# Optimization experiments

Measured on AMD Instinct MI355X. Metric: run time of the kernel, lower is better.

Reference implementation:

```python
import jax, jax.numpy as jnp
import numpy as np

DIM = 64; NFEATS = 32; DEPTH = 4; HEADS = 8; DIM_HEAD = 64
INNER = HEADS * DIM_HEAD            # 512
DI_COL = int(DIM * 4.0)             # 256
D_ROW = DIM * NFEATS                # 2048
DI_ROW = int(D_ROW * 0.5)           # 1024
B = 2048; NCAT = 16; NCONT = 16
EPS = 1e-5


def setup_inputs() -> dict:
    key = jax.random.key(0)
    ks = iter(jax.random.split(key, 32))
    def w(shape):
        return jax.random.normal(next(ks), shape, jnp.float32) * 0.02
    inp = {
        'x': jax.random.normal(next(ks), (B, NCAT, DIM), jnp.float32),
        'x_cont': jax.random.normal(next(ks), (B, NCONT, DIM), jnp.float32),
        # col-attention blocks (stacked over depth)
        'c_ln1_g': jnp.ones((DEPTH, DIM), jnp.float32),
        'c_ln1_b': jnp.zeros((DEPTH, DIM), jnp.float32),
        'c_wqkv': w((DEPTH, DIM, 3 * INNER)),
        'c_wo_w': w((DEPTH, INNER, DIM)),
        'c_wo_b': jnp.zeros((DEPTH, DIM), jnp.float32),
        'c_ln2_g': jnp.ones((DEPTH, DIM), jnp.float32),
        'c_ln2_b': jnp.zeros((DEPTH, DIM), jnp.float32),
        'c_w1': w((DEPTH, DIM, 2 * DI_COL)),
        'c_b1': jnp.zeros((DEPTH, 2 * DI_COL), jnp.float32),
        'c_w2': w((DEPTH, DI_COL, DIM)),
        'c_b2': jnp.zeros((DEPTH, DIM), jnp.float32),
        # row (intersample) blocks
        'r_ln1_g': jnp.ones((DEPTH, D_ROW), jnp.float32),
        'r_ln1_b': jnp.zeros((DEPTH, D_ROW), jnp.float32),
        'r_wqkv': w((DEPTH, D_ROW, 3 * INNER)),
        'r_wo_w': w((DEPTH, INNER, D_ROW)),
        'r_wo_b': jnp.zeros((DEPTH, D_ROW), jnp.float32),
        'r_ln2_g': jnp.ones((DEPTH, D_ROW), jnp.float32),
        'r_ln2_b': jnp.zeros((DEPTH, D_ROW), jnp.float32),
        'r_w1': w((DEPTH, D_ROW, 2 * DI_ROW)),
        'r_b1': jnp.zeros((DEPTH, 2 * DI_ROW), jnp.float32),
        'r_w2': w((DEPTH, DI_ROW, D_ROW)),
        'r_b2': jnp.zeros((DEPTH, D_ROW), jnp.float32),
    }
    return inp


def _ln(x, g, b):
    m = x.mean(-1, keepdims=True)
    v = ((x - m) ** 2).mean(-1, keepdims=True)
    return (x - m) / jnp.sqrt(v + EPS) * g + b


def _attn(x, wqkv, wo_w, wo_b):
    b, n, _ = x.shape
    q, k, v = jnp.split(x @ wqkv, 3, axis=-1)
    sp = lambda t: t.reshape(b, n, HEADS, DIM_HEAD).transpose(0, 2, 1, 3)
    q, k, v = sp(q), sp(k), sp(v)
    logits = jnp.einsum('bhid,bhjd->bhij', q, k) * (DIM_HEAD ** -0.5)
    a = jax.nn.softmax(logits, axis=-1)
    o = jnp.einsum('bhij,bhjd->bhid', a, v)
    o = o.transpose(0, 2, 1, 3).reshape(b, n, INNER)
    return o @ wo_w + wo_b


def _geglu_mlp(x, w1, b1, w2, b2):
    h = x @ w1 + b1
    a, g = jnp.split(h, 2, axis=-1)
    return (a * jax.nn.gelu(g, approximate=False)) @ w2 + b2


def _block(x, ln1g, ln1b, wqkv, wow, wob, ln2g, ln2b, w1, b1, w2, b2):
    # PreNorm(Residual(fn)): out = fn(LN(x)) + LN(x)  (residual on normalized x)
    xn = _ln(x, ln1g, ln1b)
    x = _attn(xn, wqkv, wow, wob) + xn
    xn = _ln(x, ln2g, ln2b)
    return _geglu_mlp(xn, w1, b1, w2, b2) + xn


def reference(x, x_cont,
              c_ln1_g, c_ln1_b, c_wqkv, c_wo_w, c_wo_b, c_ln2_g, c_ln2_b, c_w1, c_b1, c_w2, c_b2,
              r_ln1_g, r_ln1_b, r_wqkv, r_wo_w, r_wo_b, r_ln2_g, r_ln2_b, r_w1, r_b1, r_w2, r_b2):
    x = jnp.concatenate([x, x_cont], axis=1)  # [B, NFEATS, DIM]
    for i in range(DEPTH):
        # col: attention over features within each sample
        x = _block(x, c_ln1_g[i], c_ln1_b[i], c_wqkv[i], c_wo_w[i], c_wo_b[i],
                   c_ln2_g[i], c_ln2_b[i], c_w1[i], c_b1[i], c_w2[i], c_b2[i])
        # row: intersample attention, 'b n d -> 1 b (n d)'
        xr = x.reshape(1, B, D_ROW)
        xr = _block(xr, r_ln1_g[i], r_ln1_b[i], r_wqkv[i], r_wo_w[i], r_wo_b[i],
                    r_ln2_g[i], r_ln2_b[i], r_w1[i], r_b1[i], r_w2[i], r_b2[i])
        x = xr.reshape(B, NFEATS, DIM)
    return x
```

## Files before the change

### kernel.cpp

```cpp
#include <hip/hip_runtime.h>
#include <hip/hip_bf16.h>
#include <cstddef>

#define BD    2048
#define NF    32
#define DIMC  64
#define HEADS 8
#define DROW  2048
#define LNEPS 1e-5f

typedef __hip_bfloat16 bf16;
typedef __attribute__((ext_vector_type(8))) short short8;
typedef __attribute__((ext_vector_type(4))) float f32x4;

#define MFMA16 __builtin_amdgcn_mfma_f32_16x16x32_bf16

__device__ inline float ldin(const void* p, size_t i, int bf) {
    if (bf) return __bfloat162float(((const bf16*)p)[i]);
    return ((const float*)p)[i];
}

__device__ inline float gelu_exact(float x) {
    return 0.5f * x * (1.0f + erff(x * 0.70710678118654752f));
}

__global__ __launch_bounds__(64) void k_detect(const void* __restrict__ x,
                                               int* __restrict__ flag) {
    int i = threadIdx.x;
    size_t idx = (size_t)(2 * i) * 16384;
    unsigned short u = ((const unsigned short*)x)[idx];
    int e = (u >> 7) & 0xFF;
    int plausible = (e == 0) || (e >= 96 && e <= 132);
    unsigned long long m = __ballot(plausible);
    if (i == 0) *flag = (__popcll(m) >= 48) ? 1 : 0;
}

__global__ __launch_bounds__(256) void k_concat(const void* __restrict__ x,
                                                const void* __restrict__ xc,
                                                float* __restrict__ X,
                                                const int* __restrict__ flag) {
    const int bf = *flag;
    int i = blockIdx.x * 256 + threadIdx.x;
    int d = i & 63;
    int f = (i >> 6) & 31;
    int b = i >> 11;
    float v = (f < 16) ? ldin(x,  ((size_t)b * 16 + f) * 64 + d, bf)
                       : ldin(xc, ((size_t)b * 16 + (f - 16)) * 64 + d, bf);
    X[i] = v;
}

__global__ __launch_bounds__(256) void k_ln64(const float* __restrict__ in,
                                              float* __restrict__ out,
                                              bf16* __restrict__ outh,
                                              const void* __restrict__ g,
                                              const void* __restrict__ b,
                                              size_t eoff,
                                              const int* __restrict__ flag) {
    const int bf = *flag;
    int row  = blockIdx.x * 4 + (threadIdx.x >> 6);
    int lane = threadIdx.x & 63;
    float v = in[(size_t)row * 64 + lane];
    float s = v;
    #pragma unroll
    for (int off = 32; off; off >>= 1) s += __shfl_xor(s, off);
    float mean = s * (1.0f / 64.0f);
    float dx = v - mean;
    float s2 = dx * dx;
    #pragma unroll
    for (int off = 32; off; off >>= 1) s2 += __shfl_xor(s2, off);
    float inv = rsqrtf(s2 * (1.0f / 64.0f) + LNEPS);
    float o = dx * inv * ldin(g, eoff + lane, bf) + ldin(b, eoff + lane, bf);
    out[(size_t)row * 64 + lane]  = o;
    outh[(size_t)row * 64 + lane] = __float2bfloat16(o);
}

__global__ __launch_bounds__(256) void k_ln_row(const float* __restrict__ in,
                                                float* __restrict__ out,
                                                bf16* __restrict__ outh,
                                                const void* __restrict__ g,
                                                const void* __restrict__ b,
                                                size_t eoff,
                                                const int* __restrict__ flag) {
    const int bf = *flag;
    const int row = blockIdx.x, tid = threadIdx.x;
    __shared__ float red[4];
    const float* r = in + (size_t)row * DROW;
    float v[8];
    float s = 0.f;
    #pragma unroll
    for (int i = 0; i < 8; ++i) { v[i] = r[tid + i * 256]; s += v[i]; }
    #pragma unroll
    for (int off = 32; off; off >>= 1) s += __shfl_xor(s, off);
    if ((tid & 63) == 0) red[tid >> 6] = s;
    __syncthreads();
    float mean = (red[0] + red[1] + red[2] + red[3]) * (1.0f / DROW);
    __syncthreads();
    float s2 = 0.f;
    #pragma unroll
    for (int i = 0; i < 8; ++i) { float dx = v[i] - mean; s2 += dx * dx; }
    #pragma unroll
    for (int off = 32; off; off >>= 1) s2 += __shfl_xor(s2, off);
    if ((tid & 63) == 0) red[tid >> 6] = s2;
    __syncthreads();
    float inv = rsqrtf((red[0] + red[1] + red[2] + red[3]) * (1.0f / DROW) + LNEPS);
    #pragma unroll
    for (int i = 0; i < 8; ++i) {
        int j = tid + i * 256;
        float o = (v[i] - mean) * inv * ldin(g, eoff + j, bf) + ldin(b, eoff + j, bf);
        out[(size_t)row * DROW + j]  = o;
        outh[(size_t)row * DROW + j] = __float2bfloat16(o);
    }
}

__global__ __launch_bounds__(256) void k_castT(const void* __restrict__ in, size_t eoff,
                                               int R, int C,
                                               bf16* __restrict__ out,
                                               const int* __restrict__ flag) {
    const int bf = *flag;
    __shared__ bf16 tile[32][33];
    const int tx = threadIdx.x & 31, ty = threadIdx.x >> 5;
    const int bx = blockIdx.x, by = blockIdx.y;
    #pragma unroll
    for (int k = 0; k < 4; ++k) {
        int r = bx * 32 + ty + k * 8;
        int c = by * 32 + tx;
        tile[ty + k * 8][tx] = __float2bfloat16(ldin(in, eoff + (size_t)r * C + c, bf));
    }
    __syncthreads();
    #pragma unroll
    for (int k = 0; k < 4; ++k) {
        int oc = by * 32 + ty + k * 8;
        int orr = bx * 32 + tx;
        out[(size_t)oc * R + orr] = tile[tx][ty + k * 8];
    }
}

__global__ __launch_bounds__(256) void k_transpose_bf(const bf16* __restrict__ in, int ld,
                                                      int R, int C,
                                                      bf16* __restrict__ out) {
    __shared__ bf16 tile[32][33];
    const int tx = threadIdx.x & 31, ty = threadIdx.x >> 5;
    const int bx = blockIdx.x, by = blockIdx.y;
    #pragma unroll
    for (int k = 0; k < 4; ++k) {
        int r = bx * 32 + ty + k * 8;
        int c = by * 32 + tx;
        tile[ty + k * 8][tx] = in[(size_t)r * ld + c];
    }
    __syncthreads();
    #pragma unroll
    for (int k = 0; k < 4; ++k) {
        int oc = by * 32 + ty + k * 8;
        int orr = bx * 32 + tx;
        out[(size_t)oc * R + orr] = tile[tx][ty + k * 8];
    }
}

template <int WM, int WN, bool OBF>
__global__ __launch_bounds__(256) void k_mfma(
    int M, int N, int K,
    const bf16* __restrict__ A, int lda, long long sA,
    const bf16* __restrict__ Bt, int ldb, long long sB,
    void* __restrict__ C, int ldc, long long sC,
    float alpha,
    const void* __restrict__ bias, size_t biasOff,
    const float* __restrict__ addend, int ldadd,
    const int* __restrict__ flag)
{
    constexpr int TM = WM * 64, TN = WN * 64;
    const int z = blockIdx.z;
    A  += (size_t)z * sA;
    Bt += (size_t)z * sB;
    const int m0 = blockIdx.y * TM, n0 = blockIdx.x * TN;
    const int tid = threadIdx.x, lane = tid & 63, wave = tid >> 6;
    const int wy = wave / WN, wx = wave % WN;
    __shared__ short As[TM][72];
    __shared__ short Bs[TN][72];
    f32x4 acc[4][4] = {};
    const int row8 = tid >> 3, chunk = (tid & 7) * 8;
    for (int k0 = 0; k0 < K; k0 += 64) {
        #pragma unroll
        for (int i = 0; i < TM / 32; ++i) {
            int r = i * 32 + row8;
            *(short8*)&As[r][chunk] =
                *(const short8*)(A + (size_t)(m0 + r) * lda + k0 + chunk);
        }
        #pragma unroll
        for (int i = 0; i < TN / 32; ++i) {
            int r = i * 32 + row8;
            *(short8*)&Bs[r][chunk] =
                *(const short8*)(Bt + (size_t)(n0 + r) * ldb + k0 + chunk);
        }
        __syncthreads();
        #pragma unroll
        for (int ks = 0; ks < 64; ks += 32) {
            short8 af[4], bfr[4];
            #pragma unroll
            for (int mt = 0; mt < 4; ++mt)
                af[mt] = *(const short8*)&As[wy * 64 + mt * 16 + (lane & 15)][ks + (lane >> 4) * 8];
            #pragma unroll
            for (int nt = 0; nt < 4; ++nt)
                bfr[nt] = *(const short8*)&Bs[wx * 64 + nt * 16 + (lane & 15)][ks + (lane >> 4) * 8];
            #pragma unroll
            for (int mt = 0; mt < 4; ++mt)
                #pragma unroll
                for (int nt = 0; nt < 4; ++nt)
                    acc[mt][nt] = MFMA16(af[mt], bfr[nt], acc[mt][nt], 0, 0, 0);
        }
        __syncthreads();
    }
    const int bfl = bias ? *flag : 0;
    #pragma unroll
    for (int mt = 0; mt < 4; ++mt) {
        #pragma unroll
        for (int r = 0; r < 4; ++r) {
            int m = m0 + wy * 64 + mt * 16 + (lane >> 4) * 4 + r;
            #pragma unroll
            for (int nt = 0; nt < 4; ++nt) {
                int n = n0 + wx * 64 + nt * 16 + (lane & 15);
                float v = acc[mt][nt][r] * alpha;
                if (bias)   v += ldin(bias, biasOff + n, bfl);
                if (addend) v += addend[(size_t)m * ldadd + n];
                size_t idx = (size_t)z * sC + (size_t)m * ldc + n;
                if constexpr (OBF) ((bf16*)C)[idx] = __float2bfloat16(v);
                else               ((float*)C)[idx] = v;
            }
        }
    }
}

template <int WM, int WN>
__global__ __launch_bounds__(256) void k_mfma_sk(
    int M, int N, int KC,
    const bf16* __restrict__ A, int lda,
    const bf16* __restrict__ Bt, int ldb,
    float* __restrict__ Cp, long long pstride)
{
    constexpr int TM = WM * 64, TN = WN * 64;
    const int z = blockIdx.z;
    const int m0 = blockIdx.y * TM, n0 = blockIdx.x * TN;
    const int tid = threadIdx.x, lane = tid & 63, wave = tid >> 6;
    const int wy = wave / WN, wx = wave % WN;
    __shared__ short As[TM][72];
    __shared__ short Bs[TN][72];
    f32x4 acc[4][4] = {};
    const int row8 = tid >> 3, chunk = (tid & 7) * 8;
    const int kend = z * KC + KC;
    for (int k0 = z * KC; k0 < kend; k0 += 64) {
        #pragma unroll
        for (int i = 0; i < TM / 32; ++i) {
            int r = i * 32 + row8;
            *(short8*)&As[r][chunk] =
                *(const short8*)(A + (size_t)(m0 + r) * lda + k0 + chunk);
        }
        #pragma unroll
        for (int i = 0; i < TN / 32; ++i) {
            int r = i * 32 + row8;
            *(short8*)&Bs[r][chunk] =
                *(const short8*)(Bt + (size_t)(n0 + r) * ldb + k0 + chunk);
        }
        __syncthreads();
        #pragma unroll
        for (int ks = 0; ks < 64; ks += 32) {
            short8 af[4], bfr[4];
            #pragma unroll
            for (int mt = 0; mt < 4; ++mt)
                af[mt] = *(const short8*)&As[wy * 64 + mt * 16 + (lane & 15)][ks + (lane >> 4) * 8];
            #pragma unroll
            for (int nt = 0; nt < 4; ++nt)
                bfr[nt] = *(const short8*)&Bs[wx * 64 + nt * 16 + (lane & 15)][ks + (lane >> 4) * 8];
            #pragma unroll
            for (int mt = 0; mt < 4; ++mt)
                #pragma unroll
                for (int nt = 0; nt < 4; ++nt)
                    acc[mt][nt] = MFMA16(af[mt], bfr[nt], acc[mt][nt], 0, 0, 0);
        }
        __syncthreads();
    }
    float* Co = Cp + (size_t)z * pstride;
    #pragma unroll
    for (int mt = 0; mt < 4; ++mt)
        #pragma unroll
        for (int r = 0; r < 4; ++r) {
            int m = m0 + wy * 64 + mt * 16 + (lane >> 4) * 4 + r;
            #pragma unroll
            for (int nt = 0; nt < 4; ++nt) {
                int n = n0 + wx * 64 + nt * 16 + (lane & 15);
                Co[(size_t)m * N + n] = acc[mt][nt][r];
            }
        }
}

template <bool OBF>
__global__ __launch_bounds__(256) void k_combine(
    int KS, const float* __restrict__ P, long long pstride, int N,
    void* __restrict__ C,
    const void* __restrict__ bias, size_t biasOff,
    const float* __restrict__ addend,
    const int* __restrict__ flag)
{
    int i = blockIdx.x * 256 + threadIdx.x;
    float v = 0.f;
    for (int z = 0; z < KS; ++z) v += P[(size_t)z * pstride + i];
    if (bias)   v += ldin(bias, biasOff + (size_t)(i % N), bias ? *flag : 0);
    if (addend) v += addend[i];
    if constexpr (OBF) ((bf16*)C)[i] = __float2bfloat16(v);
    else               ((float*)C)[i] = v;
}

__device__ inline void proj_tile(const short8 xa[2][2], const bf16* __restrict__ wbase,
                                 int l15, int quad, f32x4 c[2][4]) {
    #pragma unroll
    for (int nt = 0; nt < 4; ++nt) {
        short8 b0 = *(const short8*)(wbase + (size_t)(nt * 16 + l15) * 64 + quad * 8);
        short8 b1 = *(const short8*)(wbase + (size_t)(nt * 16 + l15) * 64 + 32 + quad * 8);
        #pragma unroll
        for (int mt = 0; mt < 2; ++mt) {
            c[mt][nt] = MFMA16(xa[mt][0], b0, c[mt][nt], 0, 0, 0);
            c[mt][nt] = MFMA16(xa[mt][1], b1, c[mt][nt], 0, 0, 0);
        }
    }
}

__global__ __launch_bounds__(256) void k_col_qkv_attn(
    const bf16* __restrict__ Xh, const bf16* __restrict__ Wt,
    bf16* __restrict__ Oh)
{
    __shared__ __align__(16) short bufA[4][2304];
    __shared__ __align__(16) short bufB[4][2304];
    const int tid = threadIdx.x, lane = tid & 63, wave = tid >> 6;
    const int task = blockIdx.x * 4 + wave;
    const int s = task >> 3, h = task & 7;
    const int l15 = lane & 15, quad = lane >> 4;
    short* A  = bufA[wave];
    short* Bb = bufB[wave];

    short8 xa[2][2];
    #pragma unroll
    for (int mt = 0; mt < 2; ++mt)
        #pragma unroll
        for (int kc = 0; kc < 2; ++kc)
            xa[mt][kc] = *(const short8*)(Xh + (size_t)(s * 32 + mt * 16 + l15) * 64 + kc * 32 + quad * 8);

    {
        f32x4 c[2][4] = {};
        proj_tile(xa, Wt + (size_t)(h * 64) * 64, l15, quad, c);
        #pragma unroll
        for (int mt = 0; mt < 2; ++mt)
            #pragma unroll
            for (int nt = 0; nt < 4; ++nt)
                #pragma unroll
                for (int r = 0; r < 4; ++r)
                    *(bf16*)&A[(mt * 16 + quad * 4 + r) * 72 + nt * 16 + l15] =
                        __float2bfloat16(c[mt][nt][r]);
    }
    {
        f32x4 c[2][4] = {};
        proj_tile(xa, Wt + (size_t)(512 + h * 64) * 64, l15, quad, c);
        #pragma unroll
        for (int mt = 0; mt < 2; ++mt)
            #pragma unroll
            for (int nt = 0; nt < 4; ++nt)
                #pragma unroll
                for (int r = 0; r < 4; ++r)
                    *(bf16*)&Bb[(mt * 16 + quad * 4 + r) * 72 + nt * 16 + l15] =
                        __float2bfloat16(c[mt][nt][r]);
    }
    f32x4 S[2][2] = {};
    #pragma unroll
    for (int mt = 0; mt < 2; ++mt) {
        short8 qa0 = *(const short8*)&A[(mt * 16 + l15) * 72 + quad * 8];
        short8 qa1 = *(const short8*)&A[(mt * 16 + l15) * 72 + 32 + quad * 8];
        #pragma unroll
        for (int nt = 0; nt < 2; ++nt) {
            short8 kb0 = *(const short8*)&Bb[(nt * 16 + l15) * 72 + quad * 8];
            short8 kb1 = *(const short8*)&Bb[(nt * 16 + l15) * 72 + 32 + quad * 8];
            S[mt][nt] = MFMA16(qa0, kb0, S[mt][nt], 0, 0, 0);
            S[mt][nt] = MFMA16(qa1, kb1, S[mt][nt], 0, 0, 0);
        }
    }
    {
        f32x4 c[2][4] = {};
        proj_tile(xa, Wt + (size_t)(1024 + h * 64) * 64, l15, quad, c);
        #pragma unroll
        for (int mt = 0; mt < 2; ++mt)
            #pragma unroll
            for (int nt = 0; nt < 4; ++nt)
                #pragma unroll
                for (int r = 0; r < 4; ++r)
                    *(bf16*)&Bb[(nt * 16 + l15) * 36 + mt * 16 + quad * 4 + r] =
                        __float2bfloat16(c[mt][nt][r]);
    }
    #pragma unroll
    for (int mt = 0; mt < 2; ++mt) {
        #pragma unroll
        for (int ri = 0; ri < 4; ++ri) {
            float l0 = S[mt][0][ri] * 0.125f, l1 = S[mt][1][ri] * 0.125f;
            float m = fmaxf(l0, l1);
            #pragma unroll
            for (int msk = 1; msk < 16; msk <<= 1) m = fmaxf(m, __shfl_xor(m, msk));
            float e0 = __expf(l0 - m), e1 = __expf(l1 - m);
            float sum = e0 + e1;
            #pragma unroll
            for (int msk = 1; msk < 16; msk <<= 1) sum += __shfl_xor(sum, msk);
            float inv = 1.0f / sum;
            int row = mt * 16 + quad * 4 + ri;
            *(bf16*)&A[row * 72 + l15]      = __float2bfloat16(e0 * inv);
            *(bf16*)&A[row * 72 + 16 + l15] = __float2bfloat16(e1 * inv);
        }
    }
    short8 pa[2];
    #pragma unroll
    for (int mt = 0; mt < 2; ++mt)
        pa[mt] = *(const short8*)&A[(mt * 16 + l15) * 72 + quad * 8];
    f32x4 O[2][4] = {};
    #pragma unroll
    for (int nt = 0; nt < 4; ++nt) {
        short8 vb = *(const short8*)&Bb[(nt * 16 + l15) * 36 + quad * 8];
        #pragma unroll
        for (int mt = 0; mt < 2; ++mt)
            O[mt][nt] = MFMA16(pa[mt], vb, O[mt][nt], 0, 0, 0);
    }
    #pragma unroll
    for (int mt = 0; mt < 2; ++mt)
        #pragma unroll
        for (int nt = 0; nt < 4; ++nt)
            #pragma unroll
            for (int ri = 0; ri < 4; ++ri) {
                size_t row = (size_t)s * 32 + mt * 16 + quad * 4 + ri;
                Oh[row * 512 + h * 64 + nt * 16 + l15] = __float2bfloat16(O[mt][nt][ri]);
            }
}

__global__ __launch_bounds__(256) void k_flash_row(
    const bf16* __restrict__ QKV, const bf16* __restrict__ Vt,
    float* __restrict__ Opart, float* __restrict__ ML)
{
    __shared__ __align__(16) short Ps[4][16][136];
    const int tid = threadIdx.x, lane = tid & 63, wave = tid >> 6;
    const int h = blockIdx.y, z = blockIdx.z;
    const int q0 = blockIdx.x * 64 + wave * 16;
    const int l15 = lane & 15, quad = lane >> 4;

    short8 qa[2];
    #pragma unroll
    for (int kc = 0; kc < 2; ++kc)
        qa[kc] = *(const short8*)(QKV + (size_t)(q0 + l15) * 1536 + h * 64 + kc * 32 + quad * 8);

    float mi[4], li[4];
    #pragma unroll
    for (int r = 0; r < 4; ++r) { mi[r] = -1e30f; li[r] = 0.f; }
    f32x4 Oa[4] = {};

    #pragma unroll
    for (int jj = 0; jj < 4; ++jj) {
        const int j = z * 4 + jj;
        f32x4 s[8] = {};
        #pragma unroll
        for (int nt = 0; nt < 8; ++nt) {
            const bf16* krow = QKV + (size_t)(j * 128 + nt * 16 + l15) * 1536 + 512 + h * 64;
            short8 kb0 = *(const short8*)(krow + quad * 8);
            short8 kb1 = *(const short8*)(krow + 32 + quad * 8);
            s[nt] = MFMA16(qa[0], kb0, s[nt], 0, 0, 0);
            s[nt] = MFMA16(qa[1], kb1, s[nt], 0, 0, 0);
        }
        #pragma unroll
        for (int r = 0; r < 4; ++r) {
            float mt = -1e30f;
            #pragma unroll
            for (int nt = 0; nt < 8; ++nt) { s[nt][r] *= 0.125f; mt = fmaxf(mt, s[nt][r]); }
            #pragma unroll
            for (int msk = 1; msk < 16; msk <<= 1) mt = fmaxf(mt, __shfl_xor(mt, msk));
            float mn = fmaxf(mi[r], mt);
            float alpha = __expf(mi[r] - mn);
            float ls = 0.f;
            #pragma unroll
            for (int nt = 0; nt < 8; ++nt) { float p = __expf(s[nt][r] - mn); s[nt][r] = p; ls += p; }
            #pragma unroll
            for (int msk = 1; msk < 16; msk <<= 1) ls += __shfl_xor(ls, msk);
            li[r] = li[r] * alpha + ls;
            mi[r] = mn;
            #pragma unroll
            for (int nt = 0; nt < 4; ++nt) Oa[nt][r] *= alpha;
            int row = quad * 4 + r;
            #pragma unroll
            for (int nt = 0; nt < 8; ++nt)
                *(bf16*)&Ps[wave][row][nt * 16 + l15] = __float2bfloat16(s[nt][r]);
        }
        short8 pa[4];
        #pragma unroll
        for (int kc = 0; kc < 4; ++kc)
            pa[kc] = *(const short8*)&Ps[wave][l15][kc * 32 + quad * 8];
        #pragma unroll
        for (int nt = 0; nt < 4; ++nt) {
            #pragma unroll
            for (int kc = 0; kc < 4; ++kc) {
                short8 vb = *(const short8*)(Vt + (size_t)(h * 64 + nt * 16 + l15) * 2048 +
                                             j * 128 + kc * 32 + quad * 8);
                Oa[nt] = MFMA16(pa[kc], vb, Oa[nt], 0, 0, 0);
            }
        }
    }
    float* Op = Opart + (size_t)z * 1048576;
    #pragma unroll
    for (int nt = 0; nt < 4; ++nt)
        #pragma unroll
        for (int r = 0; r < 4; ++r)
            Op[(size_t)(q0 + quad * 4 + r) * 512 + h * 64 + nt * 16 + l15] = Oa[nt][r];
    if (l15 == 0) {
        #pragma unroll
        for (int r = 0; r < 4; ++r) {
            int row = q0 + quad * 4 + r;
            ML[((size_t)(z * 8 + h) * 2048 + row) * 2]     = mi[r];
            ML[((size_t)(z * 8 + h) * 2048 + row) * 2 + 1] = li[r];
        }
    }
}

__global__ __launch_bounds__(256) void k_flash_combine(
    const float* __restrict__ Opart, const float* __restrict__ ML,
    bf16* __restrict__ O)
{
    int i = blockIdx.x * 256 + threadIdx.x;
    int row = i >> 9, n = i & 511, h = n >> 6;
    float m[4], l[4], M = -1e30f;
    #pragma unroll
    for (int z = 0; z < 4; ++z) {
        m[z] = ML[((size_t)(z * 8 + h) * 2048 + row) * 2];
        l[z] = ML[((size_t)(z * 8 + h) * 2048 + row) * 2 + 1];
        M = fmaxf(M, m[z]);
    }
    float num = 0.f, den = 0.f;
    #pragma unroll
    for (int z = 0; z < 4; ++z) {
        float w = __expf(m[z] - M);
        num += w * Opart[(size_t)z * 1048576 + i];
        den += w * l[z];
    }
    O[i] = __float2bfloat16(num / den);
}

__global__ __launch_bounds__(256) void k_geglu_row(const float* __restrict__ H,
                                                   bf16* __restrict__ P) {
    int i = blockIdx.x * 256 + threadIdx.x;
    int r = i >> 10, j = i & 1023;
    float a = H[(size_t)r * 2048 + j];
    float g = H[(size_t)r * 2048 + 1024 + j];
    P[i] = __float2bfloat16(a * gelu_exact(g));
}

__global__ __launch_bounds__(256) void k_geglu_col(const bf16* __restrict__ H,
                                                   bf16* __restrict__ P) {
    int i = blockIdx.x * 256 + threadIdx.x;
    int r = i >> 8, j = i & 255;
    float a = __bfloat162float(H[(size_t)r * 512 + j]);
    float g = __bfloat162float(H[(size_t)r * 512 + 256 + j]);
    P[i] = __float2bfloat16(a * gelu_exact(g));
}

__global__ __launch_bounds__(256) void k_cast_out(const float* __restrict__ X,
                                                  void* __restrict__ out,
                                                  const int* __restrict__ flag) {
    const int bf = *flag;
    int i = blockIdx.x * 256 + threadIdx.x;
    if (bf) ((bf16*)out)[i] = __float2bfloat16(X[i]);
    else    ((float*)out)[i] = X[i];
}

extern "C" void kernel_launch(void* const* d_in, const int* in_sizes, int n_in,
                              void* d_out, int out_size, void* d_ws, size_t ws_size,
                              hipStream_t stream) {
    const void* x       = d_in[0];
    const void* x_cont  = d_in[1];
    const void* c_ln1_g = d_in[2];
    const void* c_ln1_b = d_in[3];
    const void* c_wqkv  = d_in[4];
    const void* c_wo_w  = d_in[5];
    const void* c_wo_b  = d_in[6];
    const void* c_ln2_g = d_in[7];
    const void* c_ln2_b = d_in[8];
    const void* c_w1    = d_in[9];
    const void* c_b1    = d_in[10];
    const void* c_w2    = d_in[11];
    const void* c_b2    = d_in[12];
    const void* r_ln1_g = d_in[13];
    const void* r_ln1_b = d_in[14];
    const void* r_wqkv  = d_in[15];
    const void* r_wo_w  = d_in[16];
    const void* r_wo_b  = d_in[17];
    const void* r_ln2_g = d_in[18];
    const void* r_ln2_b = d_in[19];
    const void* r_w1    = d_in[20];
    const void* r_b1    = d_in[21];
    const void* r_w2    = d_in[22];
    const void* r_b2    = d_in[23];

    const size_t NX = (size_t)BD * NF * DIMC;
    float* X   = (float*)d_ws;
    float* XN  = X   + NX;
    float* ACC = XN  + NX;
    bf16* XNh  = (bf16*)(ACC + NX);
    bf16* WtR  = XNh + NX;
    bf16* WcQ  = WtR + (size_t)2048 * 2048;
    bf16* WcO  = WcQ + 98304;
    bf16* Wc1  = WcO + 32768;
    bf16* Wc2  = Wc1 + 32768;
    bf16* Sc   = Wc2 + 16384;

    bf16*  OhC  = Sc;
    float* GpCW = (float*)((char*)Sc + 67108864);
    bf16*  H1   = Sc;
    bf16*  Pc   = Sc + 33554432;
    float* GpC2 = (float*)Sc;
    bf16*  QKVhR = Sc;
    bf16*  VtR   = QKVhR + 3145728;
    bf16*  OhR   = VtR + 1048576;
    bf16*  PmR   = OhR + 1048576;
    float* Hrow  = (float*)(PmR + 2097152);
    float* GpR   = (float*)((char*)Sc + 33554432);
    float* MLp   = GpR + (size_t)4 * 1048576;

    char* scEnd = (char*)Sc + 100663296;
    int*  flag  = (int*)scEnd;
    const size_t need = (size_t)(scEnd + 64 - (char*)d_ws);
    if (ws_size < need) return;

    k_detect<<<1, 64, 0, stream>>>(x, flag);
    k_concat<<<16384, 256, 0, stream>>>(x, x_cont, X, flag);

    for (int d = 0; d < 4; ++d) {
        k_ln64<<<16384, 256, 0, stream>>>(X, XN, XNh, c_ln1_g, c_ln1_b, (size_t)d * 64, flag);
        k_castT<<<dim3(2, 48), 256, 0, stream>>>(c_wqkv, (size_t)d * 64 * 1536, 64, 1536, WcQ, flag);
        k_col_qkv_attn<<<4096, 256, 0, stream>>>(XNh, WcQ, OhC);
        k_castT<<<dim3(16, 2), 256, 0, stream>>>(c_wo_w, (size_t)d * 512 * 64, 512, 64, WcO, flag);
        k_mfma_sk<4, 1><<<dim3(1, 256, 2), 256, 0, stream>>>(
            65536, 64, 256, OhC, 512, WcO, 512, GpCW, 4194304);
        k_combine<false><<<16384, 256, 0, stream>>>(
            2, GpCW, 4194304, 64, ACC, c_wo_b, (size_t)d * 64, XN, flag);
        k_ln64<<<16384, 256, 0, stream>>>(ACC, XN, XNh, c_ln2_g, c_ln2_b, (size_t)d * 64, flag);
        k_castT<<<dim3(2, 16), 256, 0, stream>>>(c_w1, (size_t)d * 64 * 512, 64, 512, Wc1, flag);
        k_mfma<2, 2, true><<<dim3(4, 512, 1), 256, 0, stream>>>(
            65536, 512, 64, XNh, 64, 0, Wc1, 64, 0,
            H1, 512, 0, 1.0f, c_b1, (size_t)d * 512, nullptr, 0, flag);
        k_geglu_col<<<65536, 256, 0, stream>>>(H1, Pc);
        k_castT<<<dim3(8, 2), 256, 0, stream>>>(c_w2, (size_t)d * 256 * 64, 256, 64, Wc2, flag);
        k_mfma_sk<4, 1><<<dim3(1, 256, 4), 256, 0, stream>>>(
            65536, 64, 64, Pc, 256, Wc2, 256, GpC2, 4194304);
        k_combine<false><<<16384, 256, 0, stream>>>(
            4, GpC2, 4194304, 64, X, c_b2, (size_t)d * 64, XN, flag);

        k_ln_row<<<BD, 256, 0, stream>>>(X, XN, XNh, r_ln1_g, r_ln1_b, (size_t)d * DROW, flag);
        k_castT<<<dim3(64, 48), 256, 0, stream>>>(r_wqkv, (size_t)d * 2048 * 1536, 2048, 1536, WtR, flag);
        k_mfma_sk<2, 2><<<dim3(12, 16, 4), 256, 0, stream>>>(
            2048, 1536, 512, XNh, 2048, WtR, 2048, GpR, 3145728);
        k_combine<true><<<12288, 256, 0, stream>>>(
            4, GpR, 3145728, 1536, QKVhR, nullptr, 0, nullptr, flag);
        k_transpose_bf<<<dim3(64, 16), 256, 0, stream>>>(QKVhR + 1024, 1536, 2048, 512, VtR);
        k_flash_row<<<dim3(32, 8, 4), 256, 0, stream>>>(QKVhR, VtR, GpR, MLp);
        k_flash_combine<<<4096, 256, 0, stream>>>(GpR, MLp, OhR);
        k_castT<<<dim3(16, 64), 256, 0, stream>>>(r_wo_w, (size_t)d * 512 * 2048, 512, 2048, WtR, flag);
        k_mfma_sk<2, 2><<<dim3(16, 16, 4), 256, 0, stream>>>(
            2048, 2048, 128, OhR, 512, WtR, 512, GpR, 4194304);
        k_combine<false><<<16384, 256, 0, stream>>>(
            4, GpR, 4194304, 2048, ACC, r_wo_b, (size_t)d * DROW, XN, flag);
        k_ln_row<<<BD, 256, 0, stream>>>(ACC, XN, XNh, r_ln2_g, r_ln2_b, (size_t)d * DROW, flag);
        k_castT<<<dim3(64, 64), 256, 0, stream>>>(r_w1, (size_t)d * 2048 * 2048, 2048, 2048, WtR, flag);
        k_mfma_sk<2, 2><<<dim3(16, 16, 4), 256, 0, stream>>>(
            2048, 2048, 512, XNh, 2048, WtR, 2048, GpR, 4194304);
        k_combine<false><<<16384, 256, 0, stream>>>(
            4, GpR, 4194304, 2048, Hrow, r_b1, (size_t)d * 2048, nullptr, flag);
        k_geglu_row<<<8192, 256, 0, stream>>>(Hrow, PmR);
        k_castT<<<dim3(32, 64), 256, 0, stream>>>(r_w2, (size_t)d * 1024 * 2048, 1024, 2048, WtR, flag);
        k_mfma_sk<2, 2><<<dim3(16, 16, 4), 256, 0, stream>>>(
            2048, 2048, 256, PmR, 1024, WtR, 1024, GpR, 4194304);
        k_combine<false><<<16384, 256, 0, stream>>>(
            4, GpR, 4194304, 2048, X, r_b2, (size_t)d * DROW, XN, flag);
    }

    k_cast_out<<<16384, 256, 0, stream>>>(X, d_out, flag);
}
```

Measured before the change: 2.359 ms.

## Accumulate split-K GEMM partials with atomics into pre-initialized outputs

```diff
diff --git a/kernel.cpp b/kernel.cpp
--- a/kernel.cpp
+++ b/kernel.cpp
@@ -291,6 +291,67 @@
         }
 }
 
+template <int WM, int WN>
+__global__ __launch_bounds__(256) void k_mfma_at(
+    int M, int N, int KC,
+    const bf16* __restrict__ A, int lda,
+    const bf16* __restrict__ Bt, int ldb,
+    float* __restrict__ C)
+{
+    constexpr int TM = WM * 64, TN = WN * 64;
+    const int z = blockIdx.z;
+    const int m0 = blockIdx.y * TM, n0 = blockIdx.x * TN;
+    const int tid = threadIdx.x, lane = tid & 63, wave = tid >> 6;
+    const int wy = wave / WN, wx = wave % WN;
+    __shared__ short As[TM][72];
+    __shared__ short Bs[TN][72];
+    f32x4 acc[4][4] = {};
+    const int row8 = tid >> 3, chunk = (tid & 7) * 8;
+    const int kend = z * KC + KC;
+    for (int k0 = z * KC; k0 < kend; k0 += 64) {
+        #pragma unroll
+        for (int i = 0; i < TM / 32; ++i) {
+            int r = i * 32 + row8;
+            *(short8*)&As[r][chunk] =
+                *(const short8*)(A + (size_t)(m0 + r) * lda + k0 + chunk);
+        }
+        #pragma unroll
+        for (int i = 0; i < TN / 32; ++i) {
+            int r = i * 32 + row8;
+            *(short8*)&Bs[r][chunk] =
+                *(const short8*)(Bt + (size_t)(n0 + r) * ldb + k0 + chunk);
+        }
+        __syncthreads();
+        #pragma unroll
+        for (int ks = 0; ks < 64; ks += 32) {
+            short8 af[4], bfr[4];
+            #pragma unroll
+            for (int mt = 0; mt < 4; ++mt)
+                af[mt] = *(const short8*)&As[wy * 64 + mt * 16 + (lane & 15)][ks + (lane >> 4) * 8];
+            #pragma unroll
+            for (int nt = 0; nt < 4; ++nt)
+                bfr[nt] = *(const short8*)&Bs[wx * 64 + nt * 16 + (lane & 15)][ks + (lane >> 4) * 8];
+            #pragma unroll
+            for (int mt = 0; mt < 4; ++mt)
+                #pragma unroll
+                for (int nt = 0; nt < 4; ++nt)
+                    acc[mt][nt] = MFMA16(af[mt], bfr[nt], acc[mt][nt], 0, 0, 0);
+        }
+        __syncthreads();
+    }
+    #pragma unroll
+    for (int mt = 0; mt < 4; ++mt)
+        #pragma unroll
+        for (int r = 0; r < 4; ++r) {
+            int m = m0 + wy * 64 + mt * 16 + (lane >> 4) * 4 + r;
+            #pragma unroll
+            for (int nt = 0; nt < 4; ++nt) {
+                int n = n0 + wx * 64 + nt * 16 + (lane & 15);
+                unsafeAtomicAdd(&C[(size_t)m * N + n], acc[mt][nt][r]);
+            }
+        }
+}
+
 template <bool OBF>
 __global__ __launch_bounds__(256) void k_combine(
     int KS, const float* __restrict__ P, long long pstride, int N,
@@ -391,22 +452,20 @@
                     *(bf16*)&Bb[(nt * 16 + l15) * 36 + mt * 16 + quad * 4 + r] =
                         __float2bfloat16(c[mt][nt][r]);
     }
+    float inv[2][4];
     #pragma unroll
     for (int mt = 0; mt < 2; ++mt) {
         #pragma unroll
         for (int ri = 0; ri < 4; ++ri) {
-            float l0 = S[mt][0][ri] * 0.125f, l1 = S[mt][1][ri] * 0.125f;
-            float m = fmaxf(l0, l1);
-            #pragma unroll
-            for (int msk = 1; msk < 16; msk <<= 1) m = fmaxf(m, __shfl_xor(m, msk));
-            float e0 = __expf(l0 - m), e1 = __expf(l1 - m);
+            float e0 = __expf(S[mt][0][ri] * 0.125f);
+            float e1 = __expf(S[mt][1][ri] * 0.125f);
             float sum = e0 + e1;
             #pragma unroll
             for (int msk = 1; msk < 16; msk <<= 1) sum += __shfl_xor(sum, msk);
-            float inv = 1.0f / sum;
+            inv[mt][ri] = 1.0f / sum;
             int row = mt * 16 + quad * 4 + ri;
-            *(bf16*)&A[row * 72 + l15]      = __float2bfloat16(e0 * inv);
-            *(bf16*)&A[row * 72 + 16 + l15] = __float2bfloat16(e1 * inv);
+            *(bf16*)&A[row * 72 + l15]      = __float2bfloat16(e0);
+            *(bf16*)&A[row * 72 + 16 + l15] = __float2bfloat16(e1);
         }
     }
     short8 pa[2];
@@ -428,7 +487,8 @@
             #pragma unroll
             for (int ri = 0; ri < 4; ++ri) {
                 size_t row = (size_t)s * 32 + mt * 16 + quad * 4 + ri;
-                Oh[row * 512 + h * 64 + nt * 16 + l15] = __float2bfloat16(O[mt][nt][ri]);
+                Oh[row * 512 + h * 64 + nt * 16 + l15] =
+                    __float2bfloat16(O[mt][nt][ri] * inv[mt][ri]);
             }
 }
 
@@ -608,10 +668,8 @@
     bf16* Sc   = Wc2 + 16384;
 
     bf16*  OhC  = Sc;
-    float* GpCW = (float*)((char*)Sc + 67108864);
     bf16*  H1   = Sc;
     bf16*  Pc   = Sc + 33554432;
-    float* GpC2 = (float*)Sc;
     bf16*  QKVhR = Sc;
     bf16*  VtR   = QKVhR + 3145728;
     bf16*  OhR   = VtR + 1048576;
@@ -633,10 +691,10 @@
         k_castT<<<dim3(2, 48), 256, 0, stream>>>(c_wqkv, (size_t)d * 64 * 1536, 64, 1536, WcQ, flag);
         k_col_qkv_attn<<<4096, 256, 0, stream>>>(XNh, WcQ, OhC);
         k_castT<<<dim3(16, 2), 256, 0, stream>>>(c_wo_w, (size_t)d * 512 * 64, 512, 64, WcO, flag);
-        k_mfma_sk<4, 1><<<dim3(1, 256, 2), 256, 0, stream>>>(
-            65536, 64, 256, OhC, 512, WcO, 512, GpCW, 4194304);
         k_combine<false><<<16384, 256, 0, stream>>>(
-            2, GpCW, 4194304, 64, ACC, c_wo_b, (size_t)d * 64, XN, flag);
+            0, nullptr, 0, 64, ACC, c_wo_b, (size_t)d * 64, XN, flag);
+        k_mfma_at<4, 1><<<dim3(1, 256, 2), 256, 0, stream>>>(
+            65536, 64, 256, OhC, 512, WcO, 512, ACC);
         k_ln64<<<16384, 256, 0, stream>>>(ACC, XN, XNh, c_ln2_g, c_ln2_b, (size_t)d * 64, flag);
         k_castT<<<dim3(2, 16), 256, 0, stream>>>(c_w1, (size_t)d * 64 * 512, 64, 512, Wc1, flag);
         k_mfma<2, 2, true><<<dim3(4, 512, 1), 256, 0, stream>>>(
@@ -644,10 +702,10 @@
             H1, 512, 0, 1.0f, c_b1, (size_t)d * 512, nullptr, 0, flag);
         k_geglu_col<<<65536, 256, 0, stream>>>(H1, Pc);
         k_castT<<<dim3(8, 2), 256, 0, stream>>>(c_w2, (size_t)d * 256 * 64, 256, 64, Wc2, flag);
-        k_mfma_sk<4, 1><<<dim3(1, 256, 4), 256, 0, stream>>>(
-            65536, 64, 64, Pc, 256, Wc2, 256, GpC2, 4194304);
         k_combine<false><<<16384, 256, 0, stream>>>(
-            4, GpC2, 4194304, 64, X, c_b2, (size_t)d * 64, XN, flag);
+            0, nullptr, 0, 64, X, c_b2, (size_t)d * 64, XN, flag);
+        k_mfma_at<4, 1><<<dim3(1, 256, 4), 256, 0, stream>>>(
+            65536, 64, 64, Pc, 256, Wc2, 256, X);
 
         k_ln_row<<<BD, 256, 0, stream>>>(X, XN, XNh, r_ln1_g, r_ln1_b, (size_t)d * DROW, flag);
         k_castT<<<dim3(64, 48), 256, 0, stream>>>(r_wqkv, (size_t)d * 2048 * 1536, 2048, 1536, WtR, flag);
@@ -659,22 +717,22 @@
         k_flash_row<<<dim3(32, 8, 4), 256, 0, stream>>>(QKVhR, VtR, GpR, MLp);
         k_flash_combine<<<4096, 256, 0, stream>>>(GpR, MLp, OhR);
         k_castT<<<dim3(16, 64), 256, 0, stream>>>(r_wo_w, (size_t)d * 512 * 2048, 512, 2048, WtR, flag);
-        k_mfma_sk<2, 2><<<dim3(16, 16, 4), 256, 0, stream>>>(
-            2048, 2048, 128, OhR, 512, WtR, 512, GpR, 4194304);
         k_combine<false><<<16384, 256, 0, stream>>>(
-            4, GpR, 4194304, 2048, ACC, r_wo_b, (size_t)d * DROW, XN, flag);
+            0, nullptr, 0, 2048, ACC, r_wo_b, (size_t)d * DROW, XN, flag);
+        k_mfma_at<2, 2><<<dim3(16, 16, 4), 256, 0, stream>>>(
+            2048, 2048, 128, OhR, 512, WtR, 512, ACC);
         k_ln_row<<<BD, 256, 0, stream>>>(ACC, XN, XNh, r_ln2_g, r_ln2_b, (size_t)d * DROW, flag);
         k_castT<<<dim3(64, 64), 256, 0, stream>>>(r_w1, (size_t)d * 2048 * 2048, 2048, 2048, WtR, flag);
-        k_mfma_sk<2, 2><<<dim3(16, 16, 4), 256, 0, stream>>>(
-            2048, 2048, 512, XNh, 2048, WtR, 2048, GpR, 4194304);
         k_combine<false><<<16384, 256, 0, stream>>>(
-            4, GpR, 4194304, 2048, Hrow, r_b1, (size_t)d * 2048, nullptr, flag);
+            0, nullptr, 0, 2048, Hrow, r_b1, (size_t)d * 2048, nullptr, flag);
+        k_mfma_at<2, 2><<<dim3(16, 16, 4), 256, 0, stream>>>(
+            2048, 2048, 512, XNh, 2048, WtR, 2048, Hrow);
         k_geglu_row<<<8192, 256, 0, stream>>>(Hrow, PmR);
         k_castT<<<dim3(32, 64), 256, 0, stream>>>(r_w2, (size_t)d * 1024 * 2048, 1024, 2048, WtR, flag);
-        k_mfma_sk<2, 2><<<dim3(16, 16, 4), 256, 0, stream>>>(
-            2048, 2048, 256, PmR, 1024, WtR, 1024, GpR, 4194304);
         k_combine<false><<<16384, 256, 0, stream>>>(
-            4, GpR, 4194304, 2048, X, r_b2, (size_t)d * DROW, XN, flag);
+            0, nullptr, 0, 2048, X, r_b2, (size_t)d * DROW, XN, flag);
+        k_mfma_at<2, 2><<<dim3(16, 16, 4), 256, 0, stream>>>(
+            2048, 2048, 256, PmR, 1024, WtR, 1024, X);
     }
 
     k_cast_out<<<16384, 256, 0, stream>>>(X, d_out, flag);
```

New measurement: 2.812 ms. 1.19x slower.

## Fuse column-block output projection and GEGLU MLP into dedicated wave-level kernels

Applied to the files above, without the earlier changes.

```diff
diff --git a/kernel.cpp b/kernel.cpp
--- a/kernel.cpp
+++ b/kernel.cpp
@@ -153,79 +153,6 @@
         int oc = by * 32 + ty + k * 8;
         int orr = bx * 32 + tx;
         out[(size_t)oc * R + orr] = tile[tx][ty + k * 8];
-    }
-}
-
-template <int WM, int WN, bool OBF>
-__global__ __launch_bounds__(256) void k_mfma(
-    int M, int N, int K,
-    const bf16* __restrict__ A, int lda, long long sA,
-    const bf16* __restrict__ Bt, int ldb, long long sB,
-    void* __restrict__ C, int ldc, long long sC,
-    float alpha,
-    const void* __restrict__ bias, size_t biasOff,
-    const float* __restrict__ addend, int ldadd,
-    const int* __restrict__ flag)
-{
-    constexpr int TM = WM * 64, TN = WN * 64;
-    const int z = blockIdx.z;
-    A  += (size_t)z * sA;
-    Bt += (size_t)z * sB;
-    const int m0 = blockIdx.y * TM, n0 = blockIdx.x * TN;
-    const int tid = threadIdx.x, lane = tid & 63, wave = tid >> 6;
-    const int wy = wave / WN, wx = wave % WN;
-    __shared__ short As[TM][72];
-    __shared__ short Bs[TN][72];
-    f32x4 acc[4][4] = {};
-    const int row8 = tid >> 3, chunk = (tid & 7) * 8;
-    for (int k0 = 0; k0 < K; k0 += 64) {
-        #pragma unroll
-        for (int i = 0; i < TM / 32; ++i) {
-            int r = i * 32 + row8;
-            *(short8*)&As[r][chunk] =
-                *(const short8*)(A + (size_t)(m0 + r) * lda + k0 + chunk);
-        }
-        #pragma unroll
-        for (int i = 0; i < TN / 32; ++i) {
-            int r = i * 32 + row8;
-            *(short8*)&Bs[r][chunk] =
-                *(const short8*)(Bt + (size_t)(n0 + r) * ldb + k0 + chunk);
-        }
-        __syncthreads();
-        #pragma unroll
-        for (int ks = 0; ks < 64; ks += 32) {
-            short8 af[4], bfr[4];
-            #pragma unroll
-            for (int mt = 0; mt < 4; ++mt)
-                af[mt] = *(const short8*)&As[wy * 64 + mt * 16 + (lane & 15)][ks + (lane >> 4) * 8];
-            #pragma unroll
-            for (int nt = 0; nt < 4; ++nt)
-                bfr[nt] = *(const short8*)&Bs[wx * 64 + nt * 16 + (lane & 15)][ks + (lane >> 4) * 8];
-            #pragma unroll
-            for (int mt = 0; mt < 4; ++mt)
-                #pragma unroll
-                for (int nt = 0; nt < 4; ++nt)
-                    acc[mt][nt] = MFMA16(af[mt], bfr[nt], acc[mt][nt], 0, 0, 0);
-        }
-        __syncthreads();
-    }
-    const int bfl = bias ? *flag : 0;
-    #pragma unroll
-    for (int mt = 0; mt < 4; ++mt) {
-        #pragma unroll
-        for (int r = 0; r < 4; ++r) {
-            int m = m0 + wy * 64 + mt * 16 + (lane >> 4) * 4 + r;
-            #pragma unroll
-            for (int nt = 0; nt < 4; ++nt) {
-                int n = n0 + wx * 64 + nt * 16 + (lane & 15);
-                float v = acc[mt][nt][r] * alpha;
-                if (bias)   v += ldin(bias, biasOff + n, bfl);
-                if (addend) v += addend[(size_t)m * ldadd + n];
-                size_t idx = (size_t)z * sC + (size_t)m * ldc + n;
-                if constexpr (OBF) ((bf16*)C)[idx] = __float2bfloat16(v);
-                else               ((float*)C)[idx] = v;
-            }
-        }
     }
 }
 
@@ -391,22 +318,20 @@
                     *(bf16*)&Bb[(nt * 16 + l15) * 36 + mt * 16 + quad * 4 + r] =
                         __float2bfloat16(c[mt][nt][r]);
     }
+    float inv[2][4];
     #pragma unroll
     for (int mt = 0; mt < 2; ++mt) {
         #pragma unroll
         for (int ri = 0; ri < 4; ++ri) {
-            float l0 = S[mt][0][ri] * 0.125f, l1 = S[mt][1][ri] * 0.125f;
-            float m = fmaxf(l0, l1);
-            #pragma unroll
-            for (int msk = 1; msk < 16; msk <<= 1) m = fmaxf(m, __shfl_xor(m, msk));
-            float e0 = __expf(l0 - m), e1 = __expf(l1 - m);
+            float e0 = __expf(S[mt][0][ri] * 0.125f);
+            float e1 = __expf(S[mt][1][ri] * 0.125f);
             float sum = e0 + e1;
             #pragma unroll
             for (int msk = 1; msk < 16; msk <<= 1) sum += __shfl_xor(sum, msk);
-            float inv = 1.0f / sum;
+            inv[mt][ri] = 1.0f / sum;
             int row = mt * 16 + quad * 4 + ri;
-            *(bf16*)&A[row * 72 + l15]      = __float2bfloat16(e0 * inv);
-            *(bf16*)&A[row * 72 + 16 + l15] = __float2bfloat16(e1 * inv);
+            *(bf16*)&A[row * 72 + l15]      = __float2bfloat16(e0);
+            *(bf16*)&A[row * 72 + 16 + l15] = __float2bfloat16(e1);
         }
     }
     short8 pa[2];
@@ -428,8 +353,129 @@
             #pragma unroll
             for (int ri = 0; ri < 4; ++ri) {
                 size_t row = (size_t)s * 32 + mt * 16 + quad * 4 + ri;
-                Oh[row * 512 + h * 64 + nt * 16 + l15] = __float2bfloat16(O[mt][nt][ri]);
+                Oh[row * 512 + h * 64 + nt * 16 + l15] =
+                    __float2bfloat16(O[mt][nt][ri] * inv[mt][ri]);
             }
+}
+
+__global__ __launch_bounds__(256) void k_col_wo(
+    const bf16* __restrict__ Oh, const bf16* __restrict__ Wt,
+    const void* __restrict__ bias, size_t biasOff,
+    const float* __restrict__ XN, float* __restrict__ ACC,
+    const int* __restrict__ flag)
+{
+    const int lane = threadIdx.x & 63, wave = threadIdx.x >> 6;
+    const int rb = (blockIdx.x * 4 + wave) * 32;
+    const int l15 = lane & 15, quad = lane >> 4;
+    f32x4 acc[2][4] = {};
+    #pragma unroll 2
+    for (int kc = 0; kc < 512; kc += 32) {
+        short8 a0 = *(const short8*)(Oh + (size_t)(rb + l15) * 512 + kc + quad * 8);
+        short8 a1 = *(const short8*)(Oh + (size_t)(rb + 16 + l15) * 512 + kc + quad * 8);
+        #pragma unroll
+        for (int nt = 0; nt < 4; ++nt) {
+            short8 b = *(const short8*)(Wt + (size_t)(nt * 16 + l15) * 512 + kc + quad * 8);
+            acc[0][nt] = MFMA16(a0, b, acc[0][nt], 0, 0, 0);
+            acc[1][nt] = MFMA16(a1, b, acc[1][nt], 0, 0, 0);
+        }
+    }
+    const int bf = *flag;
+    #pragma unroll
+    for (int nt = 0; nt < 4; ++nt) {
+        float bv = ldin(bias, biasOff + nt * 16 + l15, bf);
+        #pragma unroll
+        for (int mt = 0; mt < 2; ++mt)
+            #pragma unroll
+            for (int r = 0; r < 4; ++r) {
+                size_t idx = (size_t)(rb + mt * 16 + quad * 4 + r) * 64 + nt * 16 + l15;
+                ACC[idx] = acc[mt][nt][r] + bv + XN[idx];
+            }
+    }
+}
+
+__global__ __launch_bounds__(256) void k_col_mlp(
+    const bf16* __restrict__ Xh,
+    const bf16* __restrict__ W1t,
+    const bf16* __restrict__ W2t,
+    const void* __restrict__ b1, size_t b1Off,
+    const void* __restrict__ b2, size_t b2Off,
+    const float* __restrict__ XN, float* __restrict__ Xout,
+    const int* __restrict__ flag)
+{
+    __shared__ __align__(16) short Pl[4][32][72];
+    const int lane = threadIdx.x & 63, wave = threadIdx.x >> 6;
+    const int rb = (blockIdx.x * 4 + wave) * 32;
+    const int l15 = lane & 15, quad = lane >> 4;
+    const int bf = *flag;
+    short (*P)[72] = Pl[wave];
+
+    short8 xa[2][2];
+    #pragma unroll
+    for (int mt = 0; mt < 2; ++mt)
+        #pragma unroll
+        for (int kc = 0; kc < 2; ++kc)
+            xa[mt][kc] = *(const short8*)(Xh + (size_t)(rb + mt * 16 + l15) * 64 + kc * 32 + quad * 8);
+
+    f32x4 xacc[2][4] = {};
+    #pragma unroll
+    for (int jc = 0; jc < 256; jc += 64) {
+        f32x4 ca[2][4] = {}, cg[2][4] = {};
+        #pragma unroll
+        for (int nt = 0; nt < 4; ++nt) {
+            const bf16* wa = W1t + (size_t)(jc + nt * 16 + l15) * 64;
+            short8 a0 = *(const short8*)(wa + quad * 8);
+            short8 a1 = *(const short8*)(wa + 32 + quad * 8);
+            const bf16* wg = W1t + (size_t)(256 + jc + nt * 16 + l15) * 64;
+            short8 g0 = *(const short8*)(wg + quad * 8);
+            short8 g1 = *(const short8*)(wg + 32 + quad * 8);
+            #pragma unroll
+            for (int mt = 0; mt < 2; ++mt) {
+                ca[mt][nt] = MFMA16(xa[mt][0], a0, ca[mt][nt], 0, 0, 0);
+                ca[mt][nt] = MFMA16(xa[mt][1], a1, ca[mt][nt], 0, 0, 0);
+                cg[mt][nt] = MFMA16(xa[mt][0], g0, cg[mt][nt], 0, 0, 0);
+                cg[mt][nt] = MFMA16(xa[mt][1], g1, cg[mt][nt], 0, 0, 0);
+            }
+        }
+        #pragma unroll
+        for (int nt = 0; nt < 4; ++nt) {
+            float ba = ldin(b1, b1Off + jc + nt * 16 + l15, bf);
+            float bg = ldin(b1, b1Off + 256 + jc + nt * 16 + l15, bf);
+            #pragma unroll
+            for (int mt = 0; mt < 2; ++mt)
+                #pragma unroll
+                for (int r = 0; r < 4; ++r) {
+                    float p = (ca[mt][nt][r] + ba) * gelu_exact(cg[mt][nt][r] + bg);
+                    *(bf16*)&P[mt * 16 + quad * 4 + r][nt * 16 + l15] = __float2bfloat16(p);
+                }
+        }
+        short8 p0[2], p1[2];
+        #pragma unroll
+        for (int mt = 0; mt < 2; ++mt) {
+            p0[mt] = *(const short8*)&P[mt * 16 + l15][quad * 8];
+            p1[mt] = *(const short8*)&P[mt * 16 + l15][32 + quad * 8];
+        }
+        #pragma unroll
+        for (int nt = 0; nt < 4; ++nt) {
+            short8 w0 = *(const short8*)(W2t + (size_t)(nt * 16 + l15) * 256 + jc + quad * 8);
+            short8 w1 = *(const short8*)(W2t + (size_t)(nt * 16 + l15) * 256 + jc + 32 + quad * 8);
+            #pragma unroll
+            for (int mt = 0; mt < 2; ++mt) {
+                xacc[mt][nt] = MFMA16(p0[mt], w0, xacc[mt][nt], 0, 0, 0);
+                xacc[mt][nt] = MFMA16(p1[mt], w1, xacc[mt][nt], 0, 0, 0);
+            }
+        }
+    }
+    #pragma unroll
+    for (int nt = 0; nt < 4; ++nt) {
+        float bv = ldin(b2, b2Off + nt * 16 + l15, bf);
+        #pragma unroll
+        for (int mt = 0; mt < 2; ++mt)
+            #pragma unroll
+            for (int r = 0; r < 4; ++r) {
+                size_t idx = (size_t)(rb + mt * 16 + quad * 4 + r) * 64 + nt * 16 + l15;
+                Xout[idx] = xacc[mt][nt][r] + bv + XN[idx];
+            }
+    }
 }
 
 __global__ __launch_bounds__(256) void k_flash_row(
@@ -546,15 +592,6 @@
     int r = i >> 10, j = i & 1023;
     float a = H[(size_t)r * 2048 + j];
     float g = H[(size_t)r * 2048 + 1024 + j];
-    P[i] = __float2bfloat16(a * gelu_exact(g));
-}
-
-__global__ __launch_bounds__(256) void k_geglu_col(const bf16* __restrict__ H,
-                                                   bf16* __restrict__ P) {
-    int i = blockIdx.x * 256 + threadIdx.x;
-    int r = i >> 8, j = i & 255;
-    float a = __bfloat162float(H[(size_t)r * 512 + j]);
-    float g = __bfloat162float(H[(size_t)r * 512 + 256 + j]);
     P[i] = __float2bfloat16(a * gelu_exact(g));
 }
 
@@ -608,10 +645,6 @@
     bf16* Sc   = Wc2 + 16384;
 
     bf16*  OhC  = Sc;
-    float* GpCW = (float*)((char*)Sc + 67108864);
-    bf16*  H1   = Sc;
-    bf16*  Pc   = Sc + 33554432;
-    float* GpC2 = (float*)Sc;
     bf16*  QKVhR = Sc;
     bf16*  VtR   = QKVhR + 3145728;
     bf16*  OhR   = VtR + 1048576;
@@ -633,21 +666,13 @@
         k_castT<<<dim3(2, 48), 256, 0, stream>>>(c_wqkv, (size_t)d * 64 * 1536, 64, 1536, WcQ, flag);
         k_col_qkv_attn<<<4096, 256, 0, stream>>>(XNh, WcQ, OhC);
         k_castT<<<dim3(16, 2), 256, 0, stream>>>(c_wo_w, (size_t)d * 512 * 64, 512, 64, WcO, flag);
-        k_mfma_sk<4, 1><<<dim3(1, 256, 2), 256, 0, stream>>>(
-            65536, 64, 256, OhC, 512, WcO, 512, GpCW, 4194304);
-        k_combine<false><<<16384, 256, 0, stream>>>(
-            2, GpCW, 4194304, 64, ACC, c_wo_b, (size_t)d * 64, XN, flag);
+        k_col_wo<<<512, 256, 0, stream>>>(OhC, WcO, c_wo_b, (size_t)d * 64, XN, ACC, flag);
         k_ln64<<<16384, 256, 0, stream>>>(ACC, XN, XNh, c_ln2_g, c_ln2_b, (size_t)d * 64, flag);
         k_castT<<<dim3(2, 16), 256, 0, stream>>>(c_w1, (size_t)d * 64 * 512, 64, 512, Wc1, flag);
-        k_mfma<2, 2, true><<<dim3(4, 512, 1), 256, 0, stream>>>(
-            65536, 512, 64, XNh, 64, 0, Wc1, 64, 0,
-            H1, 512, 0, 1.0f, c_b1, (size_t)d * 512, nullptr, 0, flag);
-        k_geglu_col<<<65536, 256, 0, stream>>>(H1, Pc);
         k_castT<<<dim3(8, 2), 256, 0, stream>>>(c_w2, (size_t)d * 256 * 64, 256, 64, Wc2, flag);
-        k_mfma_sk<4, 1><<<dim3(1, 256, 4), 256, 0, stream>>>(
-            65536, 64, 64, Pc, 256, Wc2, 256, GpC2, 4194304);
-        k_combine<false><<<16384, 256, 0, stream>>>(
-            4, GpC2, 4194304, 64, X, c_b2, (size_t)d * 64, XN, flag);
+        k_col_mlp<<<512, 256, 0, stream>>>(XNh, Wc1, Wc2,
+                                           c_b1, (size_t)d * 512, c_b2, (size_t)d * 64,
+                                           XN, X, flag);
 
         k_ln_row<<<BD, 256, 0, stream>>>(X, XN, XNh, r_ln1_g, r_ln1_b, (size_t)d * DROW, flag);
         k_castT<<<dim3(64, 48), 256, 0, stream>>>(r_wqkv, (size_t)d * 2048 * 1536, 2048, 1536, WtR, flag);
```

New measurement: 2.107 ms. -10.7%, faster.
